# Optimization experiments

Measured on AMD Instinct MI355X. Metric: run time of the kernel, lower is better.

Reference implementation:

```python
import jax, jax.numpy as jnp
import numpy as np

FEATURE_DIM = 512
NUM_HEADS = 8
HEAD_DIM = FEATURE_DIM // NUM_HEADS


def setup_inputs() -> dict:
    key = jax.random.key(0)
    ks = jax.random.split(key, 16)
    B, N, F = 16, 768, FEATURE_DIM
    Nb = N // 3
    s = 1.0 / np.sqrt(F)
    inp = {
        "x_1": jax.random.normal(ks[0], (B, N, F), jnp.float32),
        "x_2": jax.random.normal(ks[1], (B, N, F), jnp.float32),
        "z_b": jax.random.normal(ks[2], (Nb, F), jnp.float32),
        # weights stored [in, out] (torch Linear applies x @ W.T)
        "Wqkv_i": jax.random.normal(ks[3], (F, 3 * F), jnp.float32) * s,
        "Wqkv_j": jax.random.normal(ks[4], (F, 3 * F), jnp.float32) * s,
        "Wqkv_b": jax.random.normal(ks[5], (F, 3 * F), jnp.float32) * s,
        "W_f": jax.random.normal(ks[6], (2 * F, F), jnp.float32) * s,
        "b_f": jnp.zeros((F,), jnp.float32),
        "W_m": jax.random.normal(ks[7], (F, F), jnp.float32) * s,
        "b_m": jnp.zeros((F,), jnp.float32),
        "W_QKV": jax.random.normal(ks[8], (F, 3 * F), jnp.float32) * s,
        "W_proj": jax.random.normal(ks[9], (F, F), jnp.float32) * s,
        "b_proj": jnp.zeros((F,), jnp.float32),
    }
    return inp


def reference(x_1, x_2, z_b, Wqkv_i, Wqkv_j, Wqkv_b, W_f, b_f, W_m, b_m, W_QKV, W_proj, b_proj):
    z_i, z_j = x_1, x_2
    B, N, F = z_i.shape
    Nb = z_b.shape[0]
    scale = F ** -0.5           # full-dim attention scale
    Scale = HEAD_DIM ** -0.5    # multi-head attention scale

    zb = jnp.broadcast_to((z_b * 0.2)[None], (B, Nb, F))

    def split_qkv(x, W):
        qkv = (x @ W).reshape(x.shape[0], x.shape[1], 3, F)
        return qkv[:, :, 0], qkv[:, :, 1], qkv[:, :, 2]

    _, k_i, v_i = split_qkv(z_i, Wqkv_i)
    q_j, _, _ = split_qkv(z_j, Wqkv_j)
    q_b, k_b, v_b = split_qkv(zb, Wqkv_b)

    # bottleneck cross attentions (single-head, full feature dim)
    a_ib = jax.nn.softmax(jnp.einsum('bmf,bnf->bmn', q_b, k_i) * scale, axis=-1)  # [B,Nb,N]
    a_bj = jax.nn.softmax(jnp.einsum('bnf,bmf->bnm', q_j, k_b) * scale, axis=-1)  # [B,N,Nb]

    a_ib = jnp.einsum('bmn,bnf->bmf', a_ib, v_i)  # [B,Nb,F]
    attn_up = jax.nn.softmax(jnp.einsum('bnf,bmf->bnm', z_i, a_ib) * scale, axis=-1)  # [B,N,Nb]
    a_ib = jnp.einsum('bnm,bmf->bnf', attn_up, a_ib)  # [B,N,F]
    a_bj = jnp.einsum('bnm,bmf->bnf', a_bj, v_b)      # [B,N,F]
    a_ij = (a_ib + a_bj) * 0.5

    # gated fusion
    f_ij = jax.nn.sigmoid(jnp.concatenate([a_ij, z_j], axis=-1) @ W_f + b_f)
    h_ij = jax.nn.relu(z_i + (a_ij @ W_m + b_m) * f_ij)

    # standard multi-head self-attention
    QKV = (h_ij @ W_QKV).reshape(B, N, 3, NUM_HEADS, HEAD_DIM)
    Q, K, V = [jnp.transpose(QKV[:, :, t], (0, 2, 1, 3)) for t in range(3)]  # [B,H,N,hd]
    Attn = jax.nn.softmax(jnp.einsum('bhnd,bhmd->bhnm', Q, K) * Scale, axis=-1)
    H = jnp.einsum('bhnm,bhmd->bhnd', Attn, V)
    H = jnp.transpose(H, (0, 2, 1, 3)).reshape(B, N, F)
    return H @ W_proj + b_proj
```

## Files before the change

kernel.cpp:

```cpp
#include <hip/hip_runtime.h>
#include <hip/hip_bf16.h>

typedef __attribute__((ext_vector_type(8))) short short8;
typedef __attribute__((ext_vector_type(4))) float f32x4;
typedef __hip_bfloat16 bf16;
typedef unsigned short ushort;

__device__ __forceinline__ ushort f2b(float v) {
    bf16 h = __float2bfloat16(v);
    return *reinterpret_cast<ushort*>(&h);
}
__device__ __forceinline__ float b2f(ushort u) {
    return __uint_as_float((unsigned)u << 16);
}

#define GLD16(lds, gp) __builtin_amdgcn_global_load_lds( \
    (const __attribute__((address_space(1))) void*)(gp), \
    (__attribute__((address_space(3))) void*)(lds), 16, 0, 0)

template<typename OutT, int EPI, int TM>
__global__ __launch_bounds__(256) void gemm_bf16(
    const bf16* __restrict__ A, const bf16* __restrict__ B, OutT* __restrict__ C,
    int K, int lda, int ldb, int ldc, long sA, long sB, long sC,
    float alpha, const float* __restrict__ bias,
    const float* __restrict__ e1, const float* __restrict__ e2, int eld, long sE,
    bf16* __restrict__ px, bf16* __restrict__ py)
{
    constexpr int RT = TM / 32;
    constexpr int AHW = TM * 32;
    constexpr int BHW = 128 * 32;
    __shared__ __align__(16) bf16 As[2 * AHW];
    __shared__ __align__(16) bf16 Bs[2 * BHW];

    const int t = threadIdx.x;
    const int w = t >> 6, lane = t & 63;
    const int wr = w >> 1, wc = w & 1;
    const int lr = lane & 15, kc4 = lane >> 4;
    const int qr = lane >> 2;
    const int kcr = ((lane & 3) - ((lane >> 3) & 3)) & 3;
    const int row0 = blockIdx.y * TM, col0 = blockIdx.x * 128;
    const int bz = blockIdx.z;

    const bf16* Asel = A; const bf16* Bsel = B;
    int abz = bz; long sBe = sB; int ldbe = ldb;
    if constexpr (EPI == 7) {
        if (bz >= 16) {
            Asel = (const bf16*)px; Bsel = (const bf16*)py;
            abz = bz - 16; sBe = 0; ldbe = eld;
        }
    }
    const bf16* Ab = Asel + (size_t)abz * sA + (size_t)row0 * lda;
    const bf16* Bb = Bsel + (size_t)abz * sBe + (size_t)col0 * ldbe;

    const bf16* ga0; const bf16* ga1 = nullptr;
    if constexpr (TM == 64) {
        ga0 = Ab + (size_t)(w * 16 + qr) * lda + kcr * 8;
    } else {
        ga0 = Ab + (size_t)(w * 32 + qr) * lda + kcr * 8;
        ga1 = Ab + (size_t)(w * 32 + 16 + qr) * lda + kcr * 8;
    }
    const bf16* gb0 = Bb + (size_t)(w * 32 + qr) * ldbe + kcr * 8;
    const bf16* gb1 = Bb + (size_t)(w * 32 + 16 + qr) * ldbe + kcr * 8;
    bf16* lA0; bf16* lA1 = nullptr;
    if constexpr (TM == 64) { lA0 = &As[w * 512]; }
    else                    { lA0 = &As[w * 1024]; lA1 = &As[w * 1024 + 512]; }
    bf16* lB0 = &Bs[w * 1024];
    bf16* lB1 = &Bs[w * 1024 + 512];

    f32x4 acc[RT][4] = {};

    const int cSw = ((kc4 + ((lr >> 1) & 3)) & 3) * 8;
    const bf16* ApBase = &As[(wr * (TM / 2) + lr) * 32 + cSw];
    const bf16* BpBase = &Bs[(wc * 64 + lr) * 32 + cSw];

    GLD16(lA0, ga0);
    if constexpr (TM == 128) GLD16(lA1, ga1);
    GLD16(lB0, gb0); GLD16(lB1, gb1);

    auto step = [&](int kk, int rd, int st) {
        __syncthreads();
        const int kn = kk + 32;
        if (kn < K) {
            GLD16(lA0 + st * AHW, ga0 + kn);
            if constexpr (TM == 128) GLD16(lA1 + st * AHW, ga1 + kn);
            GLD16(lB0 + st * BHW, gb0 + kn);
            GLD16(lB1 + st * BHW, gb1 + kn);
        }
        const bf16* Ap = ApBase + rd * AHW;
        const bf16* Bp = BpBase + rd * BHW;
        short8 af[RT], bfr[4];
#pragma unroll
        for (int i = 0; i < RT; ++i) af[i]  = *(const short8*)(Ap + i * 512);
#pragma unroll
        for (int j = 0; j < 4; ++j) bfr[j] = *(const short8*)(Bp + j * 512);
#pragma unroll
        for (int i = 0; i < RT; ++i)
#pragma unroll
            for (int j = 0; j < 4; ++j)
                acc[i][j] = __builtin_amdgcn_mfma_f32_16x16x32_bf16(af[i], bfr[j], acc[i][j], 0, 0, 0);
    };

    for (int k0 = 0; k0 < K; k0 += 64) {
        step(k0, 0, 1);
        step(k0 + 32, 1, 0);
    }

    if constexpr (EPI == 4) {
        const int sec = blockIdx.x >> 2;
        const int h0 = (blockIdx.x & 3) * 2;
        const int b  = blockIdx.y / 6;
        const int n0 = (blockIdx.y % 6) * TM;
        bf16* dq = (bf16*)C;
#pragma unroll
        for (int j = 0; j < 4; ++j) {
            const int col = wc * 64 + j * 16 + lr;
            const int h = h0 + (col >> 6), hd = col & 63;
            const size_t bh = (size_t)b * 8 + h;
#pragma unroll
            for (int i = 0; i < RT; ++i) {
                const int n = n0 + wr * (TM / 2) + i * 16 + kc4 * 4;
                if (sec == 2) {
                    __align__(8) ushort o[4];
#pragma unroll
                    for (int r = 0; r < 4; ++r) o[r] = f2b(acc[i][j][r]);
                    *(int2*)&py[(bh * 64 + hd) * 768 + n] = *(const int2*)o;
                } else {
                    bf16* d = (sec == 0) ? dq : px;
#pragma unroll
                    for (int r = 0; r < 4; ++r)
                        d[(bh * 768 + n + r) * 64 + hd] = __float2bfloat16(acc[i][j][r]);
                }
            }
        }
        return;
    } else if constexpr (EPI == 5) {
        const int b  = blockIdx.y / 6;
        const int n0 = (blockIdx.y % 6) * TM;
#pragma unroll
        for (int j = 0; j < 4; ++j) {
            const int col = col0 + wc * 64 + j * 16 + lr;
#pragma unroll
            for (int i = 0; i < RT; ++i) {
                const int n = n0 + wr * (TM / 2) + i * 16 + kc4 * 4;
                if (col < 512) {
#pragma unroll
                    for (int r = 0; r < 4; ++r)
                        ((bf16*)C)[((size_t)b * 768 + n + r) * 512 + col] = __float2bfloat16(acc[i][j][r]);
                } else {
                    __align__(8) ushort o[4];
#pragma unroll
                    for (int r = 0; r < 4; ++r) o[r] = f2b(acc[i][j][r]);
                    *(int2*)&py[((size_t)b * 512 + (col - 512)) * 768 + n] = *(const int2*)o;
                }
            }
        }
        return;
    }

    OutT* Cb = C + (size_t)bz * sC;
#pragma unroll
    for (int j = 0; j < 4; ++j) {
        const int col = col0 + wc * 64 + j * 16 + lr;
        const float bv = bias ? bias[col] : 0.f;
#pragma unroll
        for (int i = 0; i < RT; ++i) {
            const int rb = row0 + wr * (TM / 2) + i * 16 + kc4 * 4;
            if constexpr (EPI == 6) {
                __align__(8) ushort o[4];
#pragma unroll
                for (int r = 0; r < 4; ++r) {
                    o[r] = f2b(alpha * acc[i][j][r]);
                    Cb[(size_t)(rb + r) * ldc + col] = __float2bfloat16(alpha * acc[i][j][r]);
                }
                *(int2*)&py[(size_t)bz * sE + (size_t)col * eld + rb] = *(const int2*)o;
            } else {
#pragma unroll
                for (int r = 0; r < 4; ++r) {
                    const int row = rb + r;
                    float v = alpha * acc[i][j][r] + bv;
                    if constexpr (sizeof(OutT) == 2)
                        Cb[(size_t)row * ldc + col] = __float2bfloat16(v);
                    else
                        Cb[(size_t)row * ldc + col] = v;
                }
            }
        }
    }
}

__global__ __launch_bounds__(256) void gemm_gate(
    const bf16* __restrict__ A, const bf16* __restrict__ Bf,
    const bf16* __restrict__ Bm, bf16* __restrict__ Cout,
    const float* __restrict__ bias_f, const float* __restrict__ bias_m,
    const float* __restrict__ x1)
{
    constexpr int AHW = 64 * 32;
    constexpr int BHW = 128 * 32;
    __shared__ __align__(16) bf16 As[2 * AHW];
    __shared__ __align__(16) bf16 FsS[2 * BHW];
    __shared__ __align__(16) bf16 MsS[2 * BHW];

    const int t = threadIdx.x;
    const int w = t >> 6, lane = t & 63;
    const int wr = w >> 1, wc = w & 1;
    const int lr = lane & 15, kc4 = lane >> 4;
    const int qr = lane >> 2;
    const int kcr = ((lane & 3) - ((lane >> 3) & 3)) & 3;
    const int row0 = blockIdx.y * 64, col0 = blockIdx.x * 128;

    const bf16* ga0 = A  + (size_t)(row0 + w * 16 + qr) * 1024 + kcr * 8;
    const bf16* gf0 = Bf + (size_t)(col0 + w * 32 + qr) * 1024 + kcr * 8;
    const bf16* gf1 = Bf + (size_t)(col0 + w * 32 + 16 + qr) * 1024 + kcr * 8;
    const bf16* gm0 = Bm + (size_t)(col0 + w * 32 + qr) * 512 + kcr * 8;
    const bf16* gm1 = Bm + (size_t)(col0 + w * 32 + 16 + qr) * 512 + kcr * 8;
    bf16* lA0 = &As[w * 512];
    bf16* lF0 = &FsS[w * 1024]; bf16* lF1 = &FsS[w * 1024 + 512];
    bf16* lM0 = &MsS[w * 1024]; bf16* lM1 = &MsS[w * 1024 + 512];

    f32x4 acc1[2][4] = {};
    f32x4 acc2[2][4] = {};

    const int cSw = ((kc4 + ((lr >> 1) & 3)) & 3) * 8;
    const bf16* ApBase = &As[(wr * 32 + lr) * 32 + cSw];
    const bf16* FpBase = &FsS[(wc * 64 + lr) * 32 + cSw];
    const bf16* MpBase = &MsS[(wc * 64 + lr) * 32 + cSw];

    GLD16(lA0, ga0);
    GLD16(lF0, gf0); GLD16(lF1, gf1);
    GLD16(lM0, gm0); GLD16(lM1, gm1);

    auto step = [&](int kk, int rd, int st) {
        __syncthreads();
        const int kn = kk + 32;
        if (kn < 1024) {
            GLD16(lA0 + st * AHW, ga0 + kn);
            GLD16(lF0 + st * BHW, gf0 + kn);
            GLD16(lF1 + st * BHW, gf1 + kn);
            if (kn < 512) {
                GLD16(lM0 + st * BHW, gm0 + kn);
                GLD16(lM1 + st * BHW, gm1 + kn);
            }
        }
        const bf16* Ap = ApBase + rd * AHW;
        const bf16* Fp = FpBase + rd * BHW;
        short8 af[2], ff[4];
#pragma unroll
        for (int i = 0; i < 2; ++i) af[i] = *(const short8*)(Ap + i * 512);
#pragma unroll
        for (int j = 0; j < 4; ++j) ff[j] = *(const short8*)(Fp + j * 512);
#pragma unroll
        for (int i = 0; i < 2; ++i)
#pragma unroll
            for (int j = 0; j < 4; ++j)
                acc1[i][j] = __builtin_amdgcn_mfma_f32_16x16x32_bf16(af[i], ff[j], acc1[i][j], 0, 0, 0);
        if (kk < 512) {
            const bf16* Mp = MpBase + rd * BHW;
            short8 mf[4];
#pragma unroll
            for (int j = 0; j < 4; ++j) mf[j] = *(const short8*)(Mp + j * 512);
#pragma unroll
            for (int i = 0; i < 2; ++i)
#pragma unroll
                for (int j = 0; j < 4; ++j)
                    acc2[i][j] = __builtin_amdgcn_mfma_f32_16x16x32_bf16(af[i], mf[j], acc2[i][j], 0, 0, 0);
        }
    };

    for (int k0 = 0; k0 < 1024; k0 += 64) {
        step(k0, 0, 1);
        step(k0 + 32, 1, 0);
    }

#pragma unroll
    for (int j = 0; j < 4; ++j) {
        const int col = col0 + wc * 64 + j * 16 + lr;
        const float bvf = bias_f[col], bvm = bias_m[col];
#pragma unroll
        for (int i = 0; i < 2; ++i) {
            const int rb = row0 + wr * 32 + i * 16 + kc4 * 4;
#pragma unroll
            for (int r = 0; r < 4; ++r) {
                const int row = rb + r;
                const float sig = 1.f / (1.f + __expf(-(acc1[i][j][r] + bvf)));
                const float rr = x1[(size_t)row * 512 + col] + (acc2[i][j][r] + bvm) * sig;
                Cout[(size_t)row * 512 + col] = __float2bfloat16(rr > 0.f ? rr : 0.f);
            }
        }
    }
}

template<typename TI, int NSRC>
__global__ __launch_bounds__(256) void k_transpose(
    const TI* __restrict__ s0, const TI* __restrict__ s1,
    const TI* __restrict__ s2, const TI* __restrict__ s3,
    bf16* __restrict__ dst, int src_ld, int dst_ld, long sSrc, long sDst,
    int rep, long repStride)
{
    __shared__ float tile[64][65];
    const int t = threadIdx.x;
    const int c0 = blockIdx.x * 64, r0 = blockIdx.y * 64;
    const int z = blockIdx.z;
    const TI* src = s0;
    if (NSRC > 1) src = (z == 0) ? s0 : (z == 1) ? s1 : (z == 2) ? s2 : s3;
    {
        const int r = t >> 2, cq = (t & 3) * 16;
        const TI* sp = src + (size_t)z * sSrc + (size_t)(r0 + r) * src_ld + c0 + cq;
        if constexpr (sizeof(TI) == 4) {
#pragma unroll
            for (int u = 0; u < 16; u += 4) {
                float4 v = *(const float4*)((const float*)sp + u);
                tile[r][cq + u]     = v.x; tile[r][cq + u + 1] = v.y;
                tile[r][cq + u + 2] = v.z; tile[r][cq + u + 3] = v.w;
            }
        } else {
            const ushort* up = (const ushort*)sp;
            union { short8 v; ushort u[8]; } p0, p1;
            p0.v = *(const short8*)up; p1.v = *(const short8*)(up + 8);
#pragma unroll
            for (int u = 0; u < 8; ++u) {
                tile[r][cq + u]     = b2f(p0.u[u]);
                tile[r][cq + 8 + u] = b2f(p1.u[u]);
            }
        }
    }
    __syncthreads();
    const int c = t >> 2, rq = (t & 3) * 16;
    __align__(16) ushort ob[16];
#pragma unroll
    for (int u = 0; u < 16; ++u) ob[u] = f2b(tile[rq + u][c]);
    for (int rp = 0; rp < rep; ++rp) {
        bf16* dp = dst + (size_t)rp * repStride + (size_t)z * sDst + (size_t)(c0 + c) * dst_ld + r0 + rq;
        *(int4*)dp       = *(const int4*)&ob[0];
        *(int4*)(dp + 8) = *(const int4*)&ob[8];
    }
}

__global__ __launch_bounds__(256) void k_cast3(const float* __restrict__ x1,
    const float* __restrict__ x2, const float* __restrict__ zb,
    bf16* __restrict__ d1, bf16* __restrict__ d2, bf16* __restrict__ d3)
{
    const int z = blockIdx.z;
    const float* src; bf16* dst; int ld; float scale; int n;
    if (z == 0)      { src = x1; dst = d1; ld = 512;  scale = 1.f;  n = 6291456; }
    else if (z == 1) { src = x2; dst = d2; ld = 1024; scale = 1.f;  n = 6291456; }
    else             { src = zb; dst = d3; ld = 512;  scale = 0.2f; n = 131072;  }
    int i = (blockIdx.x * 256 + threadIdx.x) * 8;
    if (i >= n) return;
    float4 a = *(const float4*)(src + i), b = *(const float4*)(src + i + 4);
    __align__(16) ushort o[8];
    o[0] = f2b(a.x * scale); o[1] = f2b(a.y * scale); o[2] = f2b(a.z * scale); o[3] = f2b(a.w * scale);
    o[4] = f2b(b.x * scale); o[5] = f2b(b.y * scale); o[6] = f2b(b.z * scale); o[7] = f2b(b.w * scale);
    int row = i >> 9, col = i & 511;
    *(int4*)(dst + (size_t)row * ld + col) = *(const int4*)o;
}

template<int COLS, int MODE>
__global__ __launch_bounds__(256) void softmax_wave(const float* __restrict__ X,
                                                    bf16* __restrict__ Y)
{
    const int wv = threadIdx.x >> 6, lane = threadIdx.x & 63;
    const long row = (long)blockIdx.x * 4 + wv;
    const float* src = X + row * COLS;
    constexpr int V = COLS / 64;
    float v[V];
#pragma unroll
    for (int i = 0; i < V; ++i) v[i] = src[lane + i * 64];
    float m = v[0];
#pragma unroll
    for (int i = 1; i < V; ++i) m = fmaxf(m, v[i]);
#pragma unroll
    for (int o = 32; o; o >>= 1) m = fmaxf(m, __shfl_xor(m, o));
    float s = 0.f;
#pragma unroll
    for (int i = 0; i < V; ++i) { v[i] = __expf(v[i] - m); s += v[i]; }
#pragma unroll
    for (int o = 32; o; o >>= 1) s += __shfl_xor(s, o);
    const float inv = 1.f / s;
    bf16* dst;
    if constexpr (MODE == 0) {
        dst = Y + row * COLS;
    } else {
        const int z = (int)(row / 768), mm = (int)(row % 768);
        dst = Y + ((size_t)(z & 15) * 768 + mm) * 512 + (z >> 4) * 256;
    }
#pragma unroll
    for (int i = 0; i < V; ++i) dst[lane + i * 64] = __float2bfloat16(v[i] * inv);
}

__global__ __launch_bounds__(256) void mhsa_flash_mfma(
    const bf16* __restrict__ Qb, const bf16* __restrict__ Kb,
    const bf16* __restrict__ VT, bf16* __restrict__ Hout)
{
    constexpr int LD = 72;
    __shared__ __align__(16) ushort Qs[64 * LD];
    __shared__ __align__(16) ushort Ks[64 * LD];
    __shared__ __align__(16) ushort Vt[64 * LD];
    __shared__ __align__(16) ushort Ps[64 * LD];

    const int t = threadIdx.x;
    const int w = t >> 6, lane = t & 63;
    const int l16 = lane & 15, q4 = lane >> 4;
    const int h = blockIdx.x, b = blockIdx.y, qt = blockIdx.z;
    const size_t bh = (size_t)b * 8 + h;
    const ushort* qbase = (const ushort*)Qb + bh * 768 * 64;
    const ushort* kbase = (const ushort*)Kb + bh * 768 * 64;
    const ushort* vbase = (const ushort*)VT + bh * 64 * 768;

    const int r = t >> 2, c0 = (t & 3) * 16;

    {
        const ushort* src = qbase + (size_t)(qt * 64 + r) * 64 + c0;
        *(int4*)&Qs[r * LD + c0]     = *(const int4*)src;
        *(int4*)&Qs[r * LD + c0 + 8] = *(const int4*)(src + 8);
    }

    int4 ka0, ka1, va0, va1;
    {
        const ushort* ks = kbase + (size_t)r * 64 + c0;
        ka0 = *(const int4*)ks; ka1 = *(const int4*)(ks + 8);
        const ushort* vs = vbase + (size_t)r * 768 + c0;
        va0 = *(const int4*)vs; va1 = *(const int4*)(vs + 8);
    }
    __syncthreads();

    short8 qf0 = *(const short8*)&Qs[(w * 16 + l16) * LD + q4 * 8];
    short8 qf1 = *(const short8*)&Qs[(w * 16 + l16) * LD + 32 + q4 * 8];

    float lsum[4] = {0.f, 0.f, 0.f, 0.f};
    f32x4 acc[4] = {};

    for (int kt = 0; kt < 12; ++kt) {
        if (kt) __syncthreads();
        *(int4*)&Ks[r * LD + c0]     = ka0;
        *(int4*)&Ks[r * LD + c0 + 8] = ka1;
        *(int4*)&Vt[r * LD + c0]     = va0;
        *(int4*)&Vt[r * LD + c0 + 8] = va1;
        __syncthreads();

        if (kt < 11) {
            const ushort* ks = kbase + (size_t)((kt + 1) * 64 + r) * 64 + c0;
            ka0 = *(const int4*)ks; ka1 = *(const int4*)(ks + 8);
            const ushort* vs = vbase + (size_t)r * 768 + (kt + 1) * 64 + c0;
            va0 = *(const int4*)vs; va1 = *(const int4*)(vs + 8);
        }

        f32x4 s[4] = {};
#pragma unroll
        for (int nt = 0; nt < 4; ++nt) {
            short8 kf0 = *(const short8*)&Ks[(nt * 16 + l16) * LD + q4 * 8];
            short8 kf1 = *(const short8*)&Ks[(nt * 16 + l16) * LD + 32 + q4 * 8];
            s[nt] = __builtin_amdgcn_mfma_f32_16x16x32_bf16(qf0, kf0, s[nt], 0, 0, 0);
            s[nt] = __builtin_amdgcn_mfma_f32_16x16x32_bf16(qf1, kf1, s[nt], 0, 0, 0);
        }

#pragma unroll
        for (int nt = 0; nt < 4; ++nt) {
#pragma unroll
            for (int e = 0; e < 4; ++e) {
                const float p = __expf(s[nt][e] * 0.125f);
                lsum[e] += p;
                Ps[(w * 16 + q4 * 4 + e) * LD + nt * 16 + l16] = f2b(p);
            }
        }

        short8 pf0 = *(const short8*)&Ps[(w * 16 + l16) * LD + q4 * 8];
        short8 pf1 = *(const short8*)&Ps[(w * 16 + l16) * LD + 32 + q4 * 8];
#pragma unroll
        for (int jt = 0; jt < 4; ++jt) {
            short8 vf0 = *(const short8*)&Vt[(jt * 16 + l16) * LD + q4 * 8];
            short8 vf1 = *(const short8*)&Vt[(jt * 16 + l16) * LD + 32 + q4 * 8];
            acc[jt] = __builtin_amdgcn_mfma_f32_16x16x32_bf16(pf0, vf0, acc[jt], 0, 0, 0);
            acc[jt] = __builtin_amdgcn_mfma_f32_16x16x32_bf16(pf1, vf1, acc[jt], 0, 0, 0);
        }
    }

    const int orow = qt * 64 + w * 16 + q4 * 4;
#pragma unroll
    for (int e = 0; e < 4; ++e) {
        float l = lsum[e];
        l += __shfl_xor(l, 1);
        l += __shfl_xor(l, 2);
        l += __shfl_xor(l, 4);
        l += __shfl_xor(l, 8);
        const float inv = 1.f / l;
        const size_t rbase = ((size_t)b * 768 + orow + e) * 512 + h * 64;
#pragma unroll
        for (int jt = 0; jt < 4; ++jt)
            Hout[rbase + jt * 16 + l16] = __float2bfloat16(acc[jt][e] * inv);
    }
}

extern "C" void kernel_launch(void* const* d_in, const int* in_sizes, int n_in,
                              void* d_out, int out_size, void* d_ws, size_t ws_size,
                              hipStream_t stream)
{
    (void)in_sizes; (void)n_in; (void)out_size; (void)ws_size;
    const float* x1     = (const float*)d_in[0];
    const float* x2     = (const float*)d_in[1];
    const float* z_b    = (const float*)d_in[2];
    const float* Wqkv_i = (const float*)d_in[3];
    const float* Wqkv_j = (const float*)d_in[4];
    const float* Wqkv_b = (const float*)d_in[5];
    const float* W_f    = (const float*)d_in[6];
    const float* b_f    = (const float*)d_in[7];
    const float* W_m    = (const float*)d_in[8];
    const float* b_m    = (const float*)d_in[9];
    const float* W_QKV  = (const float*)d_in[10];
    const float* W_proj = (const float*)d_in[11];
    const float* b_proj = (const float*)d_in[12];
    float* out = (float*)d_out;

    const float scale = 0.044194173824159216f;

    char* base = (char*)d_ws;
    size_t off = 0;
    auto alloc = [&](size_t bytes) { char* r = base + off; off += (bytes + 255) & ~(size_t)255; return r; };

    char* Rq  = alloc((size_t)3 * 25165824);
    char* R1  = Rq;
    char* R2  = Rq + 25165824;
    char* R3  = Rq + 2 * 25165824;
    char* R4  = alloc(25165824);
    bf16* Wt4     = (bf16*)alloc((size_t)4 * 1536 * 512 * 2);
    bf16* Wt_f    = (bf16*)alloc(512 * 1024 * 2);
    bf16* Wt_mp   = (bf16*)alloc((size_t)2 * 512 * 512 * 2);
    bf16* c_zb    = (bf16*)alloc(256 * 512 * 2);
    bf16* qkvb    = (bf16*)alloc(256 * 1536 * 2);
    bf16* aib0    = (bf16*)alloc((size_t)16 * 256 * 512 * 2);
    bf16* Bcat    = (bf16*)alloc((size_t)16 * 512 * 512 * 2);
    float* S      = (float*)alloc((size_t)32 * 768 * 256 * 4);
    bf16* Sb1     = (bf16*)alloc((size_t)16 * 256 * 768 * 2);
    bf16* Sb_cat  = (bf16*)alloc((size_t)16 * 768 * 512 * 2);
    bf16* c_cat   = (bf16*)alloc((size_t)12288 * 1024 * 2);
    bf16* hbuf    = (bf16*)alloc((size_t)12288 * 512 * 2);

    bf16* Wt_i = Wt4, *Wt_j = Wt4 + 1536 * 512, *Wt_b = Wt4 + 2 * 1536 * 512,
        *Wt_qkv = Wt4 + (size_t)3 * 1536 * 512;
    bf16* Wt_m = Wt_mp, *Wt_proj = Wt_mp + 512 * 512;

    bf16*  Kc   = (bf16*)R1;
    bf16*  Qb   = (bf16*)R1;
    bf16*  Kb   = (bf16*)(R1 + 12582912);
    bf16*  v_iT = (bf16*)R2;
    bf16*  VTb  = (bf16*)R2;
    bf16*  c_x1 = (bf16*)R3;
    bf16*  qj   = (bf16*)R4;   bf16* Hout = (bf16*)R4;

    auto G64 = [&](const bf16* A, const bf16* B, void* C, bool outBf,
                   int M, int N, int K, int lda, int ldb, int ldc,
                   long sA, long sB, long sC, int batch, float alpha, const float* bias) {
        dim3 grid(N / 128, M / 64, batch);
        if (outBf) gemm_bf16<bf16, 0, 64><<<grid, 256, 0, stream>>>(A, B, (bf16*)C, K, lda, ldb, ldc, sA, sB, sC, alpha, bias, nullptr, nullptr, 0, 0, nullptr, nullptr);
        else       gemm_bf16<float, 0, 64><<<grid, 256, 0, stream>>>(A, B, (float*)C, K, lda, ldb, ldc, sA, sB, sC, alpha, bias, nullptr, nullptr, 0, 0, nullptr, nullptr);
    };

    k_cast3<<<dim3(3072, 1, 3), 256, 0, stream>>>(x1, x2, z_b, c_x1, c_cat + 512, c_zb);
    k_transpose<float, 4><<<dim3(24, 8, 4), 256, 0, stream>>>(
        Wqkv_i, Wqkv_j, Wqkv_b, W_QKV, Wt4, 1536, 512, 0, 1536L * 512, 1, 0);
    k_transpose<float, 1><<<dim3(8, 16, 1), 256, 0, stream>>>(
        W_f, nullptr, nullptr, nullptr, Wt_f, 512, 1024, 0, 0, 1, 0);
    k_transpose<float, 2><<<dim3(8, 8, 2), 256, 0, stream>>>(
        W_m, W_proj, nullptr, nullptr, Wt_mp, 512, 512, 0, 512L * 512, 1, 0);

    G64(c_zb, Wt_b, qkvb, true, 256, 1536, 512, 512, 512, 1536, 0, 0, 0, 1, 1.f, nullptr);
    k_transpose<bf16, 1><<<dim3(8, 4, 1), 256, 0, stream>>>(
        qkvb + 1024, nullptr, nullptr, nullptr, Bcat + 256, 1536, 512, 0, 0, 16, 512L * 512);
    gemm_bf16<bf16, 5, 128><<<dim3(8, 96, 1), 256, 0, stream>>>(
        c_x1, Wt_i + 512 * 512, Kc, 512, 512, 512, 512, 0, 0, 0,
        1.f, nullptr, nullptr, nullptr, 0, 0, nullptr, v_iT);
    G64(c_cat + 512, Wt_j, qj, true, 12288, 512, 512, 1024, 512, 512, 0, 0, 0, 1, 1.f, nullptr);
    G64(qkvb, Kc, S, false, 256, 768, 512, 1536, 512, 768, 0, 768L * 512, 256L * 768, 16, scale, nullptr);
    softmax_wave<768, 0><<<1024, 256, 0, stream>>>(S, Sb1);
    gemm_bf16<bf16, 6, 64><<<dim3(4, 4, 16), 256, 0, stream>>>(
        Sb1, v_iT, aib0, 768, 768, 768, 512, 256L * 768, 512L * 768, 256L * 512,
        1.f, nullptr, nullptr, nullptr, 512, 512L * 512, nullptr, Bcat);
    gemm_bf16<float, 7, 64><<<dim3(2, 12, 32), 256, 0, stream>>>(
        c_x1, aib0, S, 512, 512, 512, 256, 768L * 512, 256L * 512, 768L * 256,
        scale, nullptr, nullptr, nullptr, 1536, 0, qj, qkvb + 512);
    softmax_wave<256, 1><<<6144, 256, 0, stream>>>(S, Sb_cat);
    G64(Sb_cat, Bcat, c_cat, true, 768, 512, 512, 512, 512, 1024,
        768L * 512, 512L * 512, 768L * 1024, 16, 0.5f, nullptr);
    gemm_gate<<<dim3(4, 192), 256, 0, stream>>>(c_cat, Wt_f, Wt_m, hbuf, b_f, b_m, x1);
    gemm_bf16<bf16, 4, 128><<<dim3(12, 96, 1), 256, 0, stream>>>(
        hbuf, Wt_qkv, Qb, 512, 512, 512, 0, 0, 0, 0,
        1.f, nullptr, nullptr, nullptr, 0, 0, Kb, VTb);
    mhsa_flash_mfma<<<dim3(8, 16, 12), 256, 0, stream>>>(Qb, Kb, VTb, Hout);
    G64(Hout, Wt_proj, out, false, 12288, 512, 512, 512, 512, 512, 0, 0, 0, 1, 1.f, b_proj);
}
```

Before: 401.6 us.

## Triple-buffer GEMM LDS pipeline with vmcnt waits and XCD-aware block swizzle

```diff
diff --git a/kernel.cpp b/kernel.cpp
--- a/kernel.cpp
+++ b/kernel.cpp
@@ -17,6 +17,17 @@
 #define GLD16(lds, gp) __builtin_amdgcn_global_load_lds( \
     (const __attribute__((address_space(1))) void*)(gp), \
     (__attribute__((address_space(3))) void*)(lds), 16, 0, 0)
+
+#define WAITVM(n) asm volatile("s_waitcnt vmcnt(" #n ")" ::: "memory")
+
+__device__ __forceinline__ void xcd_swizzle(int& bx, int& by) {
+    if (gridDim.z == 1 && (gridDim.y & 7) == 0) {
+        const int id = bx + gridDim.x * by;
+        const int xcd = id & 7, slot = id >> 3;
+        by = xcd * (gridDim.y >> 3) + slot / gridDim.x;
+        bx = slot - (slot / gridDim.x) * gridDim.x;
+    }
+}
 
 template<typename OutT, int EPI, int TM>
 __global__ __launch_bounds__(256) void gemm_bf16(
@@ -29,8 +40,8 @@
     constexpr int RT = TM / 32;
     constexpr int AHW = TM * 32;
     constexpr int BHW = 128 * 32;
-    __shared__ __align__(16) bf16 As[2 * AHW];
-    __shared__ __align__(16) bf16 Bs[2 * BHW];
+    __shared__ __align__(16) bf16 As[3 * AHW];
+    __shared__ __align__(16) bf16 Bs[3 * BHW];
 
     const int t = threadIdx.x;
     const int w = t >> 6, lane = t & 63;
@@ -38,7 +49,9 @@
     const int lr = lane & 15, kc4 = lane >> 4;
     const int qr = lane >> 2;
     const int kcr = ((lane & 3) - ((lane >> 3) & 3)) & 3;
-    const int row0 = blockIdx.y * TM, col0 = blockIdx.x * 128;
+    int bx = blockIdx.x, by = blockIdx.y;
+    xcd_swizzle(bx, by);
+    const int row0 = by * TM, col0 = bx * 128;
     const int bz = blockIdx.z;
 
     const bf16* Asel = A; const bf16* Bsel = B;
@@ -73,21 +86,16 @@
     const bf16* ApBase = &As[(wr * (TM / 2) + lr) * 32 + cSw];
     const bf16* BpBase = &Bs[(wc * 64 + lr) * 32 + cSw];
 
-    GLD16(lA0, ga0);
-    if constexpr (TM == 128) GLD16(lA1, ga1);
-    GLD16(lB0, gb0); GLD16(lB1, gb1);
-
-    auto step = [&](int kk, int rd, int st) {
-        __syncthreads();
-        const int kn = kk + 32;
-        if (kn < K) {
-            GLD16(lA0 + st * AHW, ga0 + kn);
-            if constexpr (TM == 128) GLD16(lA1 + st * AHW, ga1 + kn);
-            GLD16(lB0 + st * BHW, gb0 + kn);
-            GLD16(lB1 + st * BHW, gb1 + kn);
-        }
-        const bf16* Ap = ApBase + rd * AHW;
-        const bf16* Bp = BpBase + rd * BHW;
+    auto issue = [&](int chunk, int b) {
+        const int ko = chunk * 32;
+        GLD16(lA0 + b * AHW, ga0 + ko);
+        if constexpr (TM == 128) GLD16(lA1 + b * AHW, ga1 + ko);
+        GLD16(lB0 + b * BHW, gb0 + ko);
+        GLD16(lB1 + b * BHW, gb1 + ko);
+    };
+    auto compute = [&](int b) {
+        const bf16* Ap = ApBase + b * AHW;
+        const bf16* Bp = BpBase + b * BHW;
         short8 af[RT], bfr[4];
 #pragma unroll
         for (int i = 0; i < RT; ++i) af[i]  = *(const short8*)(Ap + i * 512);
@@ -100,16 +108,30 @@
                 acc[i][j] = __builtin_amdgcn_mfma_f32_16x16x32_bf16(af[i], bfr[j], acc[i][j], 0, 0, 0);
     };
 
-    for (int k0 = 0; k0 < K; k0 += 64) {
-        step(k0, 0, 1);
-        step(k0 + 32, 1, 0);
-    }
+    const int S = K >> 5;
+    issue(0, 0); issue(1, 1);
+    int cb = 0, ib = 2;
+    for (int tt = 0; tt < S - 2; ++tt) {
+        if constexpr (TM == 128) WAITVM(4); else WAITVM(3);
+        __builtin_amdgcn_s_barrier();
+        issue(tt + 2, ib);
+        compute(cb);
+        cb = (cb == 2) ? 0 : cb + 1;
+        ib = (ib == 2) ? 0 : ib + 1;
+    }
+    if constexpr (TM == 128) WAITVM(4); else WAITVM(3);
+    __builtin_amdgcn_s_barrier();
+    compute(cb);
+    cb = (cb == 2) ? 0 : cb + 1;
+    WAITVM(0);
+    __builtin_amdgcn_s_barrier();
+    compute(cb);
 
     if constexpr (EPI == 4) {
-        const int sec = blockIdx.x >> 2;
-        const int h0 = (blockIdx.x & 3) * 2;
-        const int b  = blockIdx.y / 6;
-        const int n0 = (blockIdx.y % 6) * TM;
+        const int sec = bx >> 2;
+        const int h0 = (bx & 3) * 2;
+        const int b  = by / 6;
+        const int n0 = (by % 6) * TM;
         bf16* dq = (bf16*)C;
 #pragma unroll
         for (int j = 0; j < 4; ++j) {
@@ -134,8 +156,8 @@
         }
         return;
     } else if constexpr (EPI == 5) {
-        const int b  = blockIdx.y / 6;
-        const int n0 = (blockIdx.y % 6) * TM;
+        const int b  = by / 6;
+        const int n0 = (by % 6) * TM;
 #pragma unroll
         for (int j = 0; j < 4; ++j) {
             const int col = col0 + wc * 64 + j * 16 + lr;
@@ -196,9 +218,8 @@
 {
     constexpr int AHW = 64 * 32;
     constexpr int BHW = 128 * 32;
-    __shared__ __align__(16) bf16 As[2 * AHW];
-    __shared__ __align__(16) bf16 FsS[2 * BHW];
-    __shared__ __align__(16) bf16 MsS[2 * BHW];
+    __shared__ __align__(16) bf16 As[3 * AHW];
+    __shared__ __align__(16) bf16 Bs[3 * BHW];
 
     const int t = threadIdx.x;
     const int w = t >> 6, lane = t & 63;
@@ -206,7 +227,9 @@
     const int lr = lane & 15, kc4 = lane >> 4;
     const int qr = lane >> 2;
     const int kcr = ((lane & 3) - ((lane >> 3) & 3)) & 3;
-    const int row0 = blockIdx.y * 64, col0 = blockIdx.x * 128;
+    int bx = blockIdx.x, by = blockIdx.y;
+    xcd_swizzle(bx, by);
+    const int row0 = by * 64, col0 = bx * 128;
 
     const bf16* ga0 = A  + (size_t)(row0 + w * 16 + qr) * 1024 + kcr * 8;
     const bf16* gf0 = Bf + (size_t)(col0 + w * 32 + qr) * 1024 + kcr * 8;
@@ -214,62 +237,68 @@
     const bf16* gm0 = Bm + (size_t)(col0 + w * 32 + qr) * 512 + kcr * 8;
     const bf16* gm1 = Bm + (size_t)(col0 + w * 32 + 16 + qr) * 512 + kcr * 8;
     bf16* lA0 = &As[w * 512];
-    bf16* lF0 = &FsS[w * 1024]; bf16* lF1 = &FsS[w * 1024 + 512];
-    bf16* lM0 = &MsS[w * 1024]; bf16* lM1 = &MsS[w * 1024 + 512];
+    bf16* lB0 = &Bs[w * 1024]; bf16* lB1 = &Bs[w * 1024 + 512];
 
     f32x4 acc1[2][4] = {};
     f32x4 acc2[2][4] = {};
 
     const int cSw = ((kc4 + ((lr >> 1) & 3)) & 3) * 8;
     const bf16* ApBase = &As[(wr * 32 + lr) * 32 + cSw];
-    const bf16* FpBase = &FsS[(wc * 64 + lr) * 32 + cSw];
-    const bf16* MpBase = &MsS[(wc * 64 + lr) * 32 + cSw];
-
-    GLD16(lA0, ga0);
-    GLD16(lF0, gf0); GLD16(lF1, gf1);
-    GLD16(lM0, gm0); GLD16(lM1, gm1);
-
-    auto step = [&](int kk, int rd, int st) {
-        __syncthreads();
-        const int kn = kk + 32;
-        if (kn < 1024) {
-            GLD16(lA0 + st * AHW, ga0 + kn);
-            GLD16(lF0 + st * BHW, gf0 + kn);
-            GLD16(lF1 + st * BHW, gf1 + kn);
-            if (kn < 512) {
-                GLD16(lM0 + st * BHW, gm0 + kn);
-                GLD16(lM1 + st * BHW, gm1 + kn);
-            }
-        }
-        const bf16* Ap = ApBase + rd * AHW;
-        const bf16* Fp = FpBase + rd * BHW;
-        short8 af[2], ff[4];
+    const bf16* BpBase = &Bs[(wc * 64 + lr) * 32 + cSw];
+
+    auto issue = [&](int chunk, int b) {
+        if (chunk < 32) {
+            const int ko = chunk * 32;
+            GLD16(lA0 + b * AHW, ga0 + ko);
+            GLD16(lB0 + b * BHW, gf0 + ko);
+            GLD16(lB1 + b * BHW, gf1 + ko);
+        } else {
+            const int ko = (chunk - 32) * 32;
+            GLD16(lA0 + b * AHW, ga0 + ko);
+            GLD16(lB0 + b * BHW, gm0 + ko);
+            GLD16(lB1 + b * BHW, gm1 + ko);
+        }
+    };
+    auto compute = [&](int chunk, int b) {
+        const bf16* Ap = ApBase + b * AHW;
+        const bf16* Bp = BpBase + b * BHW;
+        short8 af[2], bfv[4];
 #pragma unroll
         for (int i = 0; i < 2; ++i) af[i] = *(const short8*)(Ap + i * 512);
 #pragma unroll
-        for (int j = 0; j < 4; ++j) ff[j] = *(const short8*)(Fp + j * 512);
-#pragma unroll
-        for (int i = 0; i < 2; ++i)
-#pragma unroll
-            for (int j = 0; j < 4; ++j)
-                acc1[i][j] = __builtin_amdgcn_mfma_f32_16x16x32_bf16(af[i], ff[j], acc1[i][j], 0, 0, 0);
-        if (kk < 512) {
-            const bf16* Mp = MpBase + rd * BHW;
-            short8 mf[4];
-#pragma unroll
-            for (int j = 0; j < 4; ++j) mf[j] = *(const short8*)(Mp + j * 512);
+        for (int j = 0; j < 4; ++j) bfv[j] = *(const short8*)(Bp + j * 512);
+        if (chunk < 32) {
 #pragma unroll
             for (int i = 0; i < 2; ++i)
 #pragma unroll
                 for (int j = 0; j < 4; ++j)
-                    acc2[i][j] = __builtin_amdgcn_mfma_f32_16x16x32_bf16(af[i], mf[j], acc2[i][j], 0, 0, 0);
+                    acc1[i][j] = __builtin_amdgcn_mfma_f32_16x16x32_bf16(af[i], bfv[j], acc1[i][j], 0, 0, 0);
+        } else {
+#pragma unroll
+            for (int i = 0; i < 2; ++i)
+#pragma unroll
+                for (int j = 0; j < 4; ++j)
+                    acc2[i][j] = __builtin_amdgcn_mfma_f32_16x16x32_bf16(af[i], bfv[j], acc2[i][j], 0, 0, 0);
         }
     };
 
-    for (int k0 = 0; k0 < 1024; k0 += 64) {
-        step(k0, 0, 1);
-        step(k0 + 32, 1, 0);
-    }
+    issue(0, 0); issue(1, 1);
+    int cb = 0, ib = 2;
+    for (int tt = 0; tt < 46; ++tt) {
+        WAITVM(3);
+        __builtin_amdgcn_s_barrier();
+        issue(tt + 2, ib);
+        compute(tt, cb);
+        cb = (cb == 2) ? 0 : cb + 1;
+        ib = (ib == 2) ? 0 : ib + 1;
+    }
+    WAITVM(3);
+    __builtin_amdgcn_s_barrier();
+    compute(46, cb);
+    cb = (cb == 2) ? 0 : cb + 1;
+    WAITVM(0);
+    __builtin_amdgcn_s_barrier();
+    compute(47, cb);
 
 #pragma unroll
     for (int j = 0; j < 4; ++j) {
```

Result: no change. 401.3 us (-0.1%).
